# Performance work log

Measured on AMD Instinct MI355X. Metric: run time of the kernel, lower is better.

Reference implementation:

```python
import jax, jax.numpy as jnp
import numpy as np

B, T, E, H = 256, 256, 384, 64

def setup_inputs() -> dict:
    key = jax.random.key(0)
    ks = jax.random.split(key, 4)
    s = 1.0 / np.sqrt(E)
    return {
        "x":  jax.random.normal(ks[0], (B, T, E), dtype=jnp.float32),
        "Wq": jax.random.normal(ks[1], (E, H), dtype=jnp.float32) * s,
        "bq": jnp.zeros((H,), dtype=jnp.float32),
        "Wk": jax.random.normal(ks[2], (E, H), dtype=jnp.float32) * s,
        "bk": jnp.zeros((H,), dtype=jnp.float32),
        "Wv": jax.random.normal(ks[3], (E, H), dtype=jnp.float32) * s,
        "bv": jnp.zeros((H,), dtype=jnp.float32),
    }

def reference(x, Wq, bq, Wk, bk, Wv, bv):
    # QKV projections: [B,T,E] @ [E,H] -> [B,T,H]
    q = x @ Wq + bq
    k = x @ Wk + bk
    v = x @ Wv + bv
    # attention scores (NOTE: original has no 1/sqrt(d) scaling)
    wei = jnp.einsum('bth,bsh->bts', q, k)  # [B,T,T]
    causal = jnp.tril(jnp.ones((T, T), dtype=bool))
    wei = jnp.where(causal, wei, -jnp.inf)
    wei = jax.nn.softmax(wei, axis=-1)
    # dropout is identity in eval mode
    out = jnp.einsum('bts,bsh->bth', wei, v)  # [B,T,H]
    return out
```

## Files before the change

### kernel.cpp

```cpp
#include <hip/hip_runtime.h>
#include <math.h>

#define Bb 256
#define Tt 256
#define Ee 384
#define Hh 64

typedef __attribute__((ext_vector_type(8))) short bf16x8;
typedef __attribute__((ext_vector_type(4))) float f32x4;
typedef __attribute__((ext_vector_type(4))) unsigned int u32x4;

__device__ inline short f2bf(float f) {
    unsigned u = __float_as_uint(f);
    u += 0x7FFFu + ((u >> 16) & 1);
    return (short)(u >> 16);
}
__device__ inline float bf2f(short s) {
    return __uint_as_float(((unsigned)(unsigned short)s) << 16);
}
__device__ inline unsigned cvt_pk_bf16(float a, float b) {
    unsigned r;
    asm("v_cvt_pk_bf16_f32 %0, %1, %2" : "=v"(r) : "v"(a), "v"(b));
    return r;
}
__device__ inline float lo16f(unsigned u) { return __uint_as_float(u << 16); }
__device__ inline float hi16f(unsigned u) { return __uint_as_float(u & 0xFFFF0000u); }

#define MFMA16(a, b, c) __builtin_amdgcn_mfma_f32_16x16x32_bf16((a), (b), (c), 0, 0, 0)

#define WLO_OFF 147456

#define BB0 65536
#define K_HI 0
#define K_LO 32768
#define VF   65536
#define QH   98304
#define QL   116736
#define PBASE 98304
#define SMEM_BYTES 135168

__global__ __launch_bounds__(256) void prep_w(
    const float* __restrict__ Wq, const float* __restrict__ Wk,
    const float* __restrict__ Wv, unsigned char* __restrict__ wsp)
{
    __shared__ float wlds[32 * 66];
    const int bid = blockIdx.x;
    const int ec  = bid / 3, m = bid - ec * 3;
    const float* Wm = (m == 0) ? Wq : (m == 1 ? Wk : Wv);
    const int tid = threadIdx.x;

    const float4* src = reinterpret_cast<const float4*>(Wm + ec * 2048) + tid * 2;
    float4 a = src[0], b = src[1];
    int f = tid * 8;
    float* d = wlds + (f >> 6) * 66 + (f & 63);
    d[0] = a.x; d[1] = a.y; d[2] = a.z; d[3] = a.w;
    d[4] = b.x; d[5] = b.y; d[6] = b.z; d[7] = b.w;
    __syncthreads();

    const int tl = tid >> 6, lu = tid & 63;
    const int koct = lu >> 4, n = lu & 15;
    const int c = tl * 16 + n;
    bf16x8 hi8, lo8;
    #pragma unroll
    for (int j = 0; j < 8; ++j) {
        float v = wlds[(koct * 8 + j) * 66 + c];
        short h = f2bf(v);
        hi8[j] = h;
        lo8[j] = f2bf(v - bf2f(h));
    }
    const int frag = ec * 12 + m * 4 + tl;
    *reinterpret_cast<bf16x8*>(wsp + frag * 1024 + lu * 16) = hi8;
    *reinterpret_cast<bf16x8*>(wsp + WLO_OFF + frag * 1024 + lu * 16) = lo8;
}

__global__ __launch_bounds__(1024) void head_fused(
    const float* __restrict__ x,
    const float* __restrict__ bq, const float* __restrict__ bk,
    const float* __restrict__ bv,
    const unsigned char* __restrict__ wsp,
    float* __restrict__ out)
{
    __shared__ __align__(16) unsigned char smem[SMEM_BYTES];

    const int b    = blockIdx.x;
    const int tid  = threadIdx.x;
    const int w    = tid >> 6;
    const int lane = tid & 63;
    const int quad = lane >> 4;
    const int nl   = lane & 15;
    const bool producer = (w >= 12);
    const int rg   = w & 3;
    const int cg   = w >> 2;

    f32x4 acc[4][4];
    #pragma unroll
    for (int i = 0; i < 4; ++i)
        #pragma unroll
        for (int j = 0; j < 4; ++j) acc[i][j] = (f32x4){0,0,0,0};

    const float4* x4 = reinterpret_cast<const float4*>(x + (size_t)b * Tt * Ee);

    auto bgld = [&](int ecn) {
        int p = ecn & 1;
        int f0 = (w - 12) * 3;
        #pragma unroll
        for (int j = 0; j < 3; ++j) {
            const unsigned char* g = wsp + (size_t)(ecn * 12 + f0 + j) * 1024 + (size_t)lane * 16;
            unsigned char* dlds = smem + BB0 + p * 24576 + (f0 + j) * 1024;
            __builtin_amdgcn_global_load_lds(
                (const __attribute__((address_space(1))) unsigned*)g,
                (__attribute__((address_space(3))) unsigned*)dlds, 16, 0, 0);
            __builtin_amdgcn_global_load_lds(
                (const __attribute__((address_space(1))) unsigned*)(g + WLO_OFF),
                (__attribute__((address_space(3))) unsigned*)(dlds + 12288), 16, 0, 0);
        }
    };

    const int pt = tid & 255;
    const float4* xp = x4 + pt * 96;
    unsigned char* adst = smem + (pt >> 4) * 1024 + (pt & 15) * 16;

    auto stageA = [&](int ecsrc, int nb) {
        float4 px[8];
        const float4* xr_ = xp + ecsrc * 8;
        #pragma unroll
        for (int j = 0; j < 8; ++j) px[j] = xr_[j];
        #pragma unroll
        for (int ko = 0; ko < 4; ++ko) {
            float v0 = px[2*ko+0].x, v1 = px[2*ko+0].y,
                  v2 = px[2*ko+0].z, v3 = px[2*ko+0].w,
                  v4 = px[2*ko+1].x, v5 = px[2*ko+1].y,
                  v6 = px[2*ko+1].z, v7 = px[2*ko+1].w;
            unsigned h0 = cvt_pk_bf16(v0, v1);
            unsigned h1 = cvt_pk_bf16(v2, v3);
            unsigned h2 = cvt_pk_bf16(v4, v5);
            unsigned h3 = cvt_pk_bf16(v6, v7);
            unsigned l0 = cvt_pk_bf16(v0 - lo16f(h0), v1 - hi16f(h0));
            unsigned l1 = cvt_pk_bf16(v2 - lo16f(h1), v3 - hi16f(h1));
            unsigned l2 = cvt_pk_bf16(v4 - lo16f(h2), v5 - hi16f(h2));
            unsigned l3 = cvt_pk_bf16(v6 - lo16f(h3), v7 - hi16f(h3));
            u32x4 hv = {h0, h1, h2, h3};
            u32x4 lv = {l0, l1, l2, l3};
            *reinterpret_cast<u32x4*>(adst + nb + ko * 256) = hv;
            *reinterpret_cast<u32x4*>(adst + nb + 16384 + ko * 256) = lv;
        }
    };

    if (producer) {
        bgld(0);
        stageA(0, 0);
    }

    for (int ec = 0; ec < 12; ++ec) {
        __syncthreads();
        if (producer) {
            if (ec < 11) {
                bgld(ec + 1);
                stageA(ec + 1, (1 - (ec & 1)) * 32768);
            }
        } else {
            const int ab = (ec & 1) * 32768;
            const int bb = BB0 + (ec & 1) * 24576;
            bf16x8 bh[4], bl[4];
            #pragma unroll
            for (int ct = 0; ct < 4; ++ct) {
                int o = bb + (cg * 4 + ct) * 1024 + lane * 16;
                bh[ct] = *reinterpret_cast<bf16x8*>(smem + o);
                bl[ct] = *reinterpret_cast<bf16x8*>(smem + o + 12288);
            }
            __builtin_amdgcn_s_setprio(1);
            #pragma unroll
            for (int rt = 0; rt < 4; ++rt) {
                int ao = ab + (rg * 4 + rt) * 1024 + lane * 16;
                bf16x8 ah = *reinterpret_cast<bf16x8*>(smem + ao);
                bf16x8 al = *reinterpret_cast<bf16x8*>(smem + ao + 16384);
                #pragma unroll
                for (int ct = 0; ct < 4; ++ct) {
                    acc[rt][ct] = MFMA16(ah, bh[ct], acc[rt][ct]);
                    acc[rt][ct] = MFMA16(al, bh[ct], acc[rt][ct]);
                    acc[rt][ct] = MFMA16(ah, bl[ct], acc[rt][ct]);
                }
            }
            __builtin_amdgcn_s_setprio(0);
        }
    }
    __syncthreads();

    if (!producer) {
        const float* bias_m = (cg == 0) ? bq : (cg == 1 ? bk : bv);
        #pragma unroll
        for (int ct = 0; ct < 4; ++ct) {
            float bias = bias_m[ct * 16 + nl];
            #pragma unroll
            for (int rt = 0; rt < 4; ++rt)
                #pragma unroll
                for (int r = 0; r < 4; ++r) acc[rt][ct][r] += bias;
        }

        if (cg == 1) {
            #pragma unroll
            for (int ct = 0; ct < 4; ++ct) {
                int h = ct * 16 + nl;
                #pragma unroll
                for (int rt = 0; rt < 4; ++rt) {
                    f32x4 v = acc[rt][ct];
                    unsigned h01 = cvt_pk_bf16(v[0], v[1]);
                    unsigned h23 = cvt_pk_bf16(v[2], v[3]);
                    unsigned l01 = cvt_pk_bf16(v[0] - lo16f(h01), v[1] - hi16f(h01));
                    unsigned l23 = cvt_pk_bf16(v[2] - lo16f(h23), v[3] - hi16f(h23));
                    int a0 = ((rg * 4 + rt) * 2 + (h >> 5)) * 1024
                           + ((((h & 31) >> 3) * 16 + quad * 4) * 8 + (h & 7)) * 2;
                    *reinterpret_cast<short*>(smem + K_HI + a0)      = (short)h01;
                    *reinterpret_cast<short*>(smem + K_HI + a0 + 16) = (short)(h01 >> 16);
                    *reinterpret_cast<short*>(smem + K_HI + a0 + 32) = (short)h23;
                    *reinterpret_cast<short*>(smem + K_HI + a0 + 48) = (short)(h23 >> 16);
                    *reinterpret_cast<short*>(smem + K_LO + a0)      = (short)l01;
                    *reinterpret_cast<short*>(smem + K_LO + a0 + 16) = (short)(l01 >> 16);
                    *reinterpret_cast<short*>(smem + K_LO + a0 + 32) = (short)l23;
                    *reinterpret_cast<short*>(smem + K_LO + a0 + 48) = (short)(l23 >> 16);
                }
            }
        } else if (cg == 2) {
            #pragma unroll
            for (int ct = 0; ct < 4; ++ct) {
                int h = ct * 16 + nl;
                #pragma unroll
                for (int rt = 0; rt < 4; ++rt) {
                    f32x4 v = acc[rt][ct];
                    unsigned h01 = cvt_pk_bf16(v[0], v[1]);
                    unsigned h23 = cvt_pk_bf16(v[2], v[3]);
                    int s29 = rg * 2 + (rt >> 1);
                    int slh = (rt & 1) * 2 + (quad >> 1);
                    int sl7 = (quad & 1) * 4;
                    int a0 = (s29 * 4 + (h >> 4)) * 1024
                           + ((slh * 16 + (h & 15)) * 8 + sl7) * 2;
                    *reinterpret_cast<unsigned*>(smem + VF + a0)     = h01;
                    *reinterpret_cast<unsigned*>(smem + VF + a0 + 4) = h23;
                }
            }
        }
    }

    auto writeQhalf = [&]() {
        #pragma unroll
        for (int ct = 0; ct < 4; ++ct) {
            int col = ct * 16 + nl;
            #pragma unroll
            for (int rt = 0; rt < 4; ++rt) {
                f32x4 v = acc[rt][ct];
                unsigned h01 = cvt_pk_bf16(v[0], v[1]);
                unsigned h23 = cvt_pk_bf16(v[2], v[3]);
                unsigned l01 = cvt_pk_bf16(v[0] - lo16f(h01), v[1] - hi16f(h01));
                unsigned l23 = cvt_pk_bf16(v[2] - lo16f(h23), v[3] - hi16f(h23));
                int s0 = rg * 64 + rt * 16 + quad * 4;
                int a0 = ((s0 & 127) * 72 + col) * 2;
                *reinterpret_cast<short*>(smem + QH + a0)       = (short)h01;
                *reinterpret_cast<short*>(smem + QH + a0 + 144) = (short)(h01 >> 16);
                *reinterpret_cast<short*>(smem + QH + a0 + 288) = (short)h23;
                *reinterpret_cast<short*>(smem + QH + a0 + 432) = (short)(h23 >> 16);
                *reinterpret_cast<short*>(smem + QL + a0)       = (short)l01;
                *reinterpret_cast<short*>(smem + QL + a0 + 144) = (short)(l01 >> 16);
                *reinterpret_cast<short*>(smem + QL + a0 + 288) = (short)l23;
                *reinterpret_cast<short*>(smem + QL + a0 + 432) = (short)(l23 >> 16);
            }
        }
    };
    bf16x8 qh0, qh1, ql0, ql1;
    auto readQ = [&]() {
        int rloc = (16 * w + nl) & 127;
        int base = rloc * 144;
        qh0 = *reinterpret_cast<bf16x8*>(smem + QH + base + quad * 16);
        qh1 = *reinterpret_cast<bf16x8*>(smem + QH + base + 64 + quad * 16);
        ql0 = *reinterpret_cast<bf16x8*>(smem + QL + base + quad * 16);
        ql1 = *reinterpret_cast<bf16x8*>(smem + QL + base + 64 + quad * 16);
    };

    if (!producer && cg == 0 && rg < 2) writeQhalf();
    __syncthreads();
    if (w < 8) readQ();
    __syncthreads();
    if (!producer && cg == 0 && rg >= 2) writeQhalf();
    __syncthreads();
    if (w >= 8) readQ();
    __syncthreads();

    f32x4 oacc[4];
    #pragma unroll
    for (int i = 0; i < 4; ++i) oacc[i] = (f32x4){0,0,0,0};
    float lsum = 0.f;
    const int t0 = w * 16;
    unsigned char* pb = smem + PBASE + w * 1344;
    const int npairs = (w >> 1) + 1;

    for (int p = 0; p < npairs; ++p) {
        #pragma unroll
        for (int hf = 0; hf < 2; ++hf) {
            int st = 2 * p + hf;
            f32x4 s0 = (f32x4){0,0,0,0}, s1 = (f32x4){0,0,0,0};
            int kb = st * 2048 + lane * 16;
            bf16x8 kh0 = *reinterpret_cast<bf16x8*>(smem + K_HI + kb);
            bf16x8 kh1 = *reinterpret_cast<bf16x8*>(smem + K_HI + kb + 1024);
            bf16x8 kl0 = *reinterpret_cast<bf16x8*>(smem + K_LO + kb);
            bf16x8 kl1 = *reinterpret_cast<bf16x8*>(smem + K_LO + kb + 1024);
            s0 = MFMA16(qh0, kh0, s0);
            s1 = MFMA16(qh1, kh1, s1);
            s0 = MFMA16(ql0, kh0, s0);
            s1 = MFMA16(ql1, kh1, s1);
            s0 = MFMA16(qh0, kl0, s0);
            s1 = MFMA16(qh1, kl1, s1);
            int sg = st * 16 + nl;
            #pragma unroll
            for (int r = 0; r < 4; ++r) {
                int tg = t0 + quad * 4 + r;
                float sv = s0[r] + s1[r];
                float pv = (sg <= tg) ? __expf(sv) : 0.f;
                *reinterpret_cast<short*>(pb + ((quad * 4 + r) * 40 + hf * 16 + nl) * 2) = f2bf(pv);
            }
        }
        asm volatile("s_waitcnt lgkmcnt(0)" ::: "memory");
        bf16x8 pa = *reinterpret_cast<bf16x8*>(pb + (nl * 40 + quad * 8) * 2);
        float ls = 0.f;
        #pragma unroll
        for (int j = 0; j < 8; ++j) ls += bf2f(pa[j]);
        ls += __shfl_xor(ls, 16);
        ls += __shfl_xor(ls, 32);
        lsum += ls;
        int vb = p * 4096 + lane * 16;
        #pragma unroll
        for (int nt = 0; nt < 4; ++nt) {
            bf16x8 vf = *reinterpret_cast<bf16x8*>(smem + VF + vb + nt * 1024);
            oacc[nt] = MFMA16(pa, vf, oacc[nt]);
        }
    }

    float* lb_ = reinterpret_cast<float*>(pb + 1280);
    if (lane < 16) lb_[lane] = lsum;
    asm volatile("s_waitcnt lgkmcnt(0)" ::: "memory");
    float* ob = out + (size_t)b * Tt * Hh + (size_t)t0 * Hh;
    #pragma unroll
    for (int r = 0; r < 4; ++r) {
        float inv = 1.0f / lb_[quad * 4 + r];
        #pragma unroll
        for (int nt = 0; nt < 4; ++nt)
            ob[(quad * 4 + r) * 64 + nt * 16 + nl] = oacc[nt][r] * inv;
    }
}

extern "C" void kernel_launch(void* const* d_in, const int* in_sizes, int n_in,
                              void* d_out, int out_size, void* d_ws, size_t ws_size,
                              hipStream_t stream) {
    const float* x  = (const float*)d_in[0];
    const float* Wq = (const float*)d_in[1];
    const float* bq = (const float*)d_in[2];
    const float* Wk = (const float*)d_in[3];
    const float* bk = (const float*)d_in[4];
    const float* Wv = (const float*)d_in[5];
    const float* bv = (const float*)d_in[6];
    float* out = (float*)d_out;
    unsigned char* wsp = (unsigned char*)d_ws;
    hipLaunchKernelGGL(prep_w, dim3(36), dim3(256), 0, stream, Wq, Wk, Wv, wsp);
    hipLaunchKernelGGL(head_fused, dim3(Bb), dim3(1024), 0, stream,
                       x, bq, bk, bv, wsp, out);
}
```

Measured before the change: 184.0 us.

## Prefetch x and K fragments, interleave score MFMAs, compute row sums in registers

The producer now loads the next x chunk into registers one iteration ahead, so global-load latency overlaps the barrier and the bf16 conversion. In attention, K fragments for the next pair are prefetched from LDS, and the two key subtiles' MFMAs are interleaved with setprio hints. Row sums are computed from fp32 probabilities with shuffle reductions instead of re-reading bf16 P and staging through LDS. This also removes the explicit lgkmcnt wait, leaving only a compiler memory barrier before reading P back. The cost is extra register pressure, and the normaliser now comes from unrounded probabilities, which slightly changes numerics.

```diff
diff --git a/kernel.cpp b/kernel.cpp
--- a/kernel.cpp
+++ b/kernel.cpp
@@ -119,12 +119,14 @@
     const int pt = tid & 255;
     const float4* xp = x4 + pt * 96;
     unsigned char* adst = smem + (pt >> 4) * 1024 + (pt & 15) * 16;
-
-    auto stageA = [&](int ecsrc, int nb) {
-        float4 px[8];
+    float4 px[8];
+
+    auto loadX = [&](int ecsrc) {
         const float4* xr_ = xp + ecsrc * 8;
         #pragma unroll
         for (int j = 0; j < 8; ++j) px[j] = xr_[j];
+    };
+    auto stageWrite = [&](int nb) {
         #pragma unroll
         for (int ko = 0; ko < 4; ++ko) {
             float v0 = px[2*ko+0].x, v1 = px[2*ko+0].y,
@@ -148,7 +150,9 @@
 
     if (producer) {
         bgld(0);
-        stageA(0, 0);
+        loadX(0);
+        stageWrite(0);
+        loadX(1);
     }
 
     for (int ec = 0; ec < 12; ++ec) {
@@ -156,8 +160,9 @@
         if (producer) {
             if (ec < 11) {
                 bgld(ec + 1);
-                stageA(ec + 1, (1 - (ec & 1)) * 32768);
-            }
+                stageWrite((1 - (ec & 1)) * 32768);
+            }
+            if (ec < 10) loadX(ec + 2);
         } else {
             const int ab = (ec & 1) * 32768;
             const int bb = BB0 + (ec & 1) * 24576;
@@ -287,59 +292,81 @@
     f32x4 oacc[4];
     #pragma unroll
     for (int i = 0; i < 4; ++i) oacc[i] = (f32x4){0,0,0,0};
-    float lsum = 0.f;
+    float lsum4[4] = {0.f, 0.f, 0.f, 0.f};
     const int t0 = w * 16;
     unsigned char* pb = smem + PBASE + w * 1344;
     const int npairs = (w >> 1) + 1;
 
+    bf16x8 kA0, kA1, kA2, kA3, kB0, kB1, kB2, kB3;
+#define LDK(P) do {                                                     \
+        int kb0_ = (2 * (P)) * 2048 + lane * 16;                        \
+        kA0 = *reinterpret_cast<bf16x8*>(smem + K_HI + kb0_);           \
+        kA1 = *reinterpret_cast<bf16x8*>(smem + K_HI + kb0_ + 1024);    \
+        kA2 = *reinterpret_cast<bf16x8*>(smem + K_LO + kb0_);           \
+        kA3 = *reinterpret_cast<bf16x8*>(smem + K_LO + kb0_ + 1024);    \
+        kB0 = *reinterpret_cast<bf16x8*>(smem + K_HI + kb0_ + 2048);    \
+        kB1 = *reinterpret_cast<bf16x8*>(smem + K_HI + kb0_ + 3072);    \
+        kB2 = *reinterpret_cast<bf16x8*>(smem + K_LO + kb0_ + 2048);    \
+        kB3 = *reinterpret_cast<bf16x8*>(smem + K_LO + kb0_ + 3072);    \
+    } while (0)
+
+    LDK(0);
     for (int p = 0; p < npairs; ++p) {
-        #pragma unroll
-        for (int hf = 0; hf < 2; ++hf) {
-            int st = 2 * p + hf;
-            f32x4 s0 = (f32x4){0,0,0,0}, s1 = (f32x4){0,0,0,0};
-            int kb = st * 2048 + lane * 16;
-            bf16x8 kh0 = *reinterpret_cast<bf16x8*>(smem + K_HI + kb);
-            bf16x8 kh1 = *reinterpret_cast<bf16x8*>(smem + K_HI + kb + 1024);
-            bf16x8 kl0 = *reinterpret_cast<bf16x8*>(smem + K_LO + kb);
-            bf16x8 kl1 = *reinterpret_cast<bf16x8*>(smem + K_LO + kb + 1024);
-            s0 = MFMA16(qh0, kh0, s0);
-            s1 = MFMA16(qh1, kh1, s1);
-            s0 = MFMA16(ql0, kh0, s0);
-            s1 = MFMA16(ql1, kh1, s1);
-            s0 = MFMA16(qh0, kl0, s0);
-            s1 = MFMA16(qh1, kl1, s1);
-            int sg = st * 16 + nl;
-            #pragma unroll
-            for (int r = 0; r < 4; ++r) {
-                int tg = t0 + quad * 4 + r;
-                float sv = s0[r] + s1[r];
-                float pv = (sg <= tg) ? __expf(sv) : 0.f;
-                *reinterpret_cast<short*>(pb + ((quad * 4 + r) * 40 + hf * 16 + nl) * 2) = f2bf(pv);
-            }
-        }
-        asm volatile("s_waitcnt lgkmcnt(0)" ::: "memory");
-        bf16x8 pa = *reinterpret_cast<bf16x8*>(pb + (nl * 40 + quad * 8) * 2);
-        float ls = 0.f;
-        #pragma unroll
-        for (int j = 0; j < 8; ++j) ls += bf2f(pa[j]);
-        ls += __shfl_xor(ls, 16);
-        ls += __shfl_xor(ls, 32);
-        lsum += ls;
+        f32x4 sa0 = (f32x4){0,0,0,0}, sa1 = (f32x4){0,0,0,0};
+        f32x4 sb0 = (f32x4){0,0,0,0}, sb1 = (f32x4){0,0,0,0};
+        __builtin_amdgcn_s_setprio(1);
+        sa0 = MFMA16(qh0, kA0, sa0);  sb0 = MFMA16(qh0, kB0, sb0);
+        sa1 = MFMA16(qh1, kA1, sa1);  sb1 = MFMA16(qh1, kB1, sb1);
+        sa0 = MFMA16(ql0, kA0, sa0);  sb0 = MFMA16(ql0, kB0, sb0);
+        sa1 = MFMA16(ql1, kA1, sa1);  sb1 = MFMA16(ql1, kB1, sb1);
+        sa0 = MFMA16(qh0, kA2, sa0);  sb0 = MFMA16(qh0, kB2, sb0);
+        sa1 = MFMA16(qh1, kA3, sa1);  sb1 = MFMA16(qh1, kB3, sb1);
+        __builtin_amdgcn_s_setprio(0);
+
+        float rs[4];
+        const int sg0 = 32 * p + nl, sg1 = sg0 + 16;
+        #pragma unroll
+        for (int r = 0; r < 4; ++r) {
+            int tg = t0 + quad * 4 + r;
+            float sva = sa0[r] + sa1[r];
+            float svb = sb0[r] + sb1[r];
+            float pva = (sg0 <= tg) ? __expf(sva) : 0.f;
+            float pvb = (sg1 <= tg) ? __expf(svb) : 0.f;
+            rs[r] = pva + pvb;
+            *reinterpret_cast<short*>(pb + ((quad * 4 + r) * 40 + nl) * 2)      = f2bf(pva);
+            *reinterpret_cast<short*>(pb + ((quad * 4 + r) * 40 + 16 + nl) * 2) = f2bf(pvb);
+        }
+        asm volatile("" ::: "memory");
+        bf16x8 pa  = *reinterpret_cast<bf16x8*>(pb + (nl * 40 + quad * 8) * 2);
         int vb = p * 4096 + lane * 16;
-        #pragma unroll
-        for (int nt = 0; nt < 4; ++nt) {
-            bf16x8 vf = *reinterpret_cast<bf16x8*>(smem + VF + vb + nt * 1024);
-            oacc[nt] = MFMA16(pa, vf, oacc[nt]);
-        }
-    }
-
-    float* lb_ = reinterpret_cast<float*>(pb + 1280);
-    if (lane < 16) lb_[lane] = lsum;
-    asm volatile("s_waitcnt lgkmcnt(0)" ::: "memory");
+        bf16x8 vf0 = *reinterpret_cast<bf16x8*>(smem + VF + vb);
+        bf16x8 vf1 = *reinterpret_cast<bf16x8*>(smem + VF + vb + 1024);
+        bf16x8 vf2 = *reinterpret_cast<bf16x8*>(smem + VF + vb + 2048);
+        bf16x8 vf3 = *reinterpret_cast<bf16x8*>(smem + VF + vb + 3072);
+        if (p + 1 < npairs) LDK(p + 1);
+
+        #pragma unroll
+        for (int r = 0; r < 4; ++r) {
+            float v = rs[r];
+            v += __shfl_xor(v, 1);
+            v += __shfl_xor(v, 2);
+            v += __shfl_xor(v, 4);
+            v += __shfl_xor(v, 8);
+            lsum4[r] += v;
+        }
+        __builtin_amdgcn_s_setprio(1);
+        oacc[0] = MFMA16(pa, vf0, oacc[0]);
+        oacc[1] = MFMA16(pa, vf1, oacc[1]);
+        oacc[2] = MFMA16(pa, vf2, oacc[2]);
+        oacc[3] = MFMA16(pa, vf3, oacc[3]);
+        __builtin_amdgcn_s_setprio(0);
+    }
+#undef LDK
+
     float* ob = out + (size_t)b * Tt * Hh + (size_t)t0 * Hh;
     #pragma unroll
     for (int r = 0; r < 4; ++r) {
-        float inv = 1.0f / lb_[quad * 4 + r];
+        float inv = 1.0f / lsum4[r];
         #pragma unroll
         for (int nt = 0; nt < 4; ++nt)
             ob[(quad * 4 + r) * 64 + nt * 16 + nl] = oacc[nt][r] * inv;
```

Result: slower. 259.1 us (+40.8%).

## Prefetch x chunks into LDS via async DMA one stage ahead

Applied to the files above, without the earlier changes.

Producer warps now issue global_load_lds DMAs that fetch the raw fp32 x chunk for stage ec+2 into a dedicated LDS staging area, then read it from LDS and split it to bf16 hi/lo. Previously each chunk went through registers with a blocking global load inside the same stage. The goal is to hide global-memory latency behind the consumer MFMA work. In exchange, LDS use grows, which may reduce occupancy, and the barrier and waitcnt handling is now manual and more fragile.

```diff
diff --git a/kernel.cpp b/kernel.cpp
--- a/kernel.cpp
+++ b/kernel.cpp
@@ -31,13 +31,14 @@
 #define WLO_OFF 147456
 
 #define BB0 65536
+#define RAW 114688
 #define K_HI 0
 #define K_LO 32768
 #define VF   65536
 #define QH   98304
 #define QL   116736
 #define PBASE 98304
-#define SMEM_BYTES 135168
+#define SMEM_BYTES 147456
 
 __global__ __launch_bounds__(256) void prep_w(
     const float* __restrict__ Wq, const float* __restrict__ Wk,
@@ -120,11 +121,18 @@
     const float4* xp = x4 + pt * 96;
     unsigned char* adst = smem + (pt >> 4) * 1024 + (pt & 15) * 16;
 
-    auto stageA = [&](int ecsrc, int nb) {
-        float4 px[8];
-        const float4* xr_ = xp + ecsrc * 8;
-        #pragma unroll
-        for (int j = 0; j < 8; ++j) px[j] = xr_[j];
+    auto rawdma = [&](int ecsrc) {
+        unsigned char* rbase = smem + RAW + (w - 12) * 1024;
+        #pragma unroll
+        for (int c = 0; c < 8; ++c) {
+            __builtin_amdgcn_global_load_lds(
+                (const __attribute__((address_space(1))) unsigned*)(xp + ecsrc * 8 + c),
+                (__attribute__((address_space(3))) unsigned*)(rbase + c * 4096),
+                16, 0, 0);
+        }
+    };
+
+    auto stageWrite = [&](int nb, const float4* px) {
         #pragma unroll
         for (int ko = 0; ko < 4; ++ko) {
             float v0 = px[2*ko+0].x, v1 = px[2*ko+0].y,
@@ -146,17 +154,42 @@
         }
     };
 
+    auto readRaw = [&](float4* px) {
+        #pragma unroll
+        for (int j = 0; j < 8; ++j)
+            px[j] = *reinterpret_cast<float4*>(smem + RAW + j * 4096 + pt * 16);
+    };
+
     if (producer) {
+        rawdma(0);
+        asm volatile("s_waitcnt vmcnt(0)" ::: "memory");
+        float4 px[8];
+        readRaw(px);
+        asm volatile("s_waitcnt lgkmcnt(0)" ::: "memory");
+        __builtin_amdgcn_sched_barrier(0);
         bgld(0);
-        stageA(0, 0);
+        rawdma(1);
+        stageWrite(0, px);
+        asm volatile("s_waitcnt vmcnt(8) lgkmcnt(0)" ::: "memory");
     }
 
     for (int ec = 0; ec < 12; ++ec) {
-        __syncthreads();
+        __builtin_amdgcn_s_barrier();
+        asm volatile("" ::: "memory");
         if (producer) {
             if (ec < 11) {
+                asm volatile("s_waitcnt vmcnt(0)" ::: "memory");
+                float4 px[8];
+                readRaw(px);
+                asm volatile("s_waitcnt lgkmcnt(0)" ::: "memory");
+                __builtin_amdgcn_sched_barrier(0);
                 bgld(ec + 1);
-                stageA(ec + 1, (1 - (ec & 1)) * 32768);
+                if (ec < 10) rawdma(ec + 2);
+                stageWrite((1 - (ec & 1)) * 32768, px);
+                if (ec < 10)
+                    asm volatile("s_waitcnt vmcnt(8) lgkmcnt(0)" ::: "memory");
+                else
+                    asm volatile("s_waitcnt vmcnt(0) lgkmcnt(0)" ::: "memory");
             }
         } else {
             const int ab = (ec & 1) * 32768;
```

Result: slower. 198.7 us (+7.9%).
